# Optimization experiments

Hardware: AMD Instinct MI355X
Metric: run time of the kernel (lower is better)

The kernel has to match this reference:

```python
import jax, jax.numpy as jnp
import numpy as np

N_HEAD = 8
EPS = 1e-6  # LayerNorm2d eps


def setup_inputs() -> dict:
    key = jax.random.key(0)
    ks = jax.random.split(key, 7)
    B, C, H, W = 16, 256, 128, 128
    nh, dk, dv = N_HEAD, 32, 32
    s = 1.0 / np.sqrt(C)
    return {
        "q": jax.random.normal(ks[0], (B, C, H, W), jnp.float32),
        "k": jax.random.normal(ks[1], (B, C, H, W), jnp.float32),
        "v": jax.random.normal(ks[2], (B, C, H, W), jnp.float32),
        # 1x1 convs without bias == channel matmuls; weight shape [out_ch, in_ch]
        "wq": jax.random.normal(ks[3], (nh * dk, C), jnp.float32) * s,
        "wk": jax.random.normal(ks[4], (nh * dk, C), jnp.float32) * s,
        "wv": jax.random.normal(ks[5], (nh * dv, C), jnp.float32) * s,
        "wfc": jax.random.normal(ks[6], (C, nh * dv), jnp.float32) * (1.0 / np.sqrt(nh * dv)),
        "ln_w": jnp.ones((C,), jnp.float32),
        "ln_b": jnp.zeros((C,), jnp.float32),
        "kernel": 5,
        "pad": 2,
    }


def _forward(q, k, v, wq, wk, wv, wfc, ln_w, ln_b, kernel, pad):
    B, C, H, W = q.shape
    nh = N_HEAD
    dk = wq.shape[0] // nh
    dv = wv.shape[0] // nh
    assert kernel == 2 * pad + 1
    residual = q
    # 1x1 conv projections, split into heads: [B, nh, d, H, W]
    qh = jnp.einsum('oc,bchw->bohw', wq, q).reshape(B, nh, dk, H, W)
    kh = jnp.einsum('oc,bchw->bohw', wk, k).reshape(B, nh, dk, H, W)
    vh = jnp.einsum('oc,bchw->bohw', wv, v).reshape(B, nh, dv, H, W)
    # zero-pad spatially: out-of-bounds correlations/values are zero, matching the
    # original bilinear sampler (zeros padding) and the custom padding() helper.
    kp = jnp.pad(kh, ((0, 0), (0, 0), (0, 0), (pad, pad), (pad, pad)))
    vp = jnp.pad(vh, ((0, 0), (0, 0), (0, 0), (pad, pad), (pad, pad)))
    # local correlation volume: dot(q[i,j], k[i+dy-pad, j+dx-pad]) for the KxK window
    # (integer offsets -> bilinear sample degenerates to a gather). Never materializes
    # the full [B, HW, HW] matrix the torch code builds before sampling.
    corr = jnp.stack(
        [jnp.einsum('bncij,bncij->bnij', qh, kp[:, :, :, dy:dy + H, dx:dx + W])
         for dy in range(kernel) for dx in range(kernel)], axis=-1)  # [B,nh,H,W,K*K]
    # relu (from CorrBlock.corr), temperature = sqrt(d_k), softmax over window.
    # OOB entries are 0 (not -inf), faithfully matching the original.
    attn = jax.nn.softmax(jax.nn.relu(corr) / jnp.float32(np.sqrt(dk)), axis=-1)
    # channel attention: per-pixel weighted sum of v over the same window
    out = jnp.zeros((B, nh, dv, H, W), q.dtype)
    idx = 0
    for dy in range(kernel):
        for dx in range(kernel):
            out = out + attn[:, :, :, :, idx][:, :, None] * vp[:, :, :, dy:dy + H, dx:dx + W]
            idx += 1
    o = jnp.einsum('oc,bchw->bohw', wfc, out.reshape(B, nh * dv, H, W)) + residual
    # LayerNorm2d: normalize over channel dim per pixel
    mu = o.mean(1, keepdims=True)
    var = ((o - mu) ** 2).mean(1, keepdims=True)
    y = (o - mu) / jnp.sqrt(var + EPS)
    return ln_w[None, :, None, None] * y + ln_b[None, :, None, None]


def reference(q, k, v, wq, wk, wv, wfc, ln_w, ln_b, kernel, pad):
    return _forward(q, k, v, wq, wk, wv, wfc, ln_w, ln_b, kernel, pad)
```

## Files before the change

kernel.cpp:

```cpp
#include <hip/hip_runtime.h>
#include <hip/hip_bf16.h>

#define BATCH 16
#define CH 256
#define HH 128
#define WW 128
#define HWSZ (HH * WW)
#define NHEAD 8
#define DHEAD 32
#define PW 132
#define PPIX (132 * 132)
#define ROWS 264
#define ASTR 40

typedef __attribute__((ext_vector_type(8))) short bf16x8;
typedef __attribute__((ext_vector_type(4))) float f32x4;
typedef _Float16 h2v __attribute__((ext_vector_type(2)));

__device__ __forceinline__ unsigned short f2h(float f) {
    _Float16 h = (_Float16)f;
    return __builtin_bit_cast(unsigned short, h);
}
__device__ __forceinline__ unsigned pkbf(float a, float b) {
    __hip_bfloat162_raw r = __hip_bfloat162_raw(__float22bfloat162_rn(make_float2(a, b)));
    return (unsigned)r.x | ((unsigned)r.y << 16);
}
__device__ __forceinline__ int swzc(int row, int chunk) { return chunk ^ ((row >> 2) & 7); }

#if __has_builtin(__builtin_amdgcn_fdot2)
#define DOT2(a, b, c) __builtin_amdgcn_fdot2((a), (b), (c), false)
#else
#define DOT2(a, b, c) ((c) + (float)(a)[0] * (float)(b)[0] + (float)(a)[1] * (float)(b)[1])
#endif

__global__ __launch_bounds__(256)
void zpad_kernel(unsigned short* __restrict__ kpad, unsigned short* __restrict__ vpad)
{
    int bid = blockIdx.x;
    unsigned short* dst = ((bid & 1) ? vpad : kpad) + (size_t)(bid >> 1) * PPIX * DHEAD;
    const uint4 z = {0u, 0u, 0u, 0u};
    for (int i = threadIdx.x; i < 1040; i += 256) {
        int row, col;
        if (i < 264)      { row = i / 132; col = i - row * 132; }
        else if (i < 528) { int j = i - 264; int r = j / 132; row = 130 + r; col = j - r * 132; }
        else              { int j = i - 528; row = 2 + (j >> 2); int c = j & 3; col = (c < 2) ? c : (128 + c); }
        uint4* p = reinterpret_cast<uint4*>(dst + (size_t)(row * PW + col) * DHEAD);
        p[0] = z; p[1] = z; p[2] = z; p[3] = z;
    }
}

__global__ __launch_bounds__(256)
void prep_kernel(const float* __restrict__ wq, const float* __restrict__ wk,
                 const float* __restrict__ wv, const float* __restrict__ wfc,
                 unsigned short* __restrict__ wb)
{
    const float* src = (blockIdx.y == 0) ? wq : (blockIdx.y == 1) ? wk
                     : (blockIdx.y == 2) ? wv : wfc;
    unsigned short* dst = wb + blockIdx.y * 65536;
    int e = (blockIdx.x * 256 + threadIdx.x) * 8;
    const float4* s = reinterpret_cast<const float4*>(src + e);
    float4 a = s[0], c = s[1];
    uint4 u;
    u.x = pkbf(a.x, a.y); u.y = pkbf(a.z, a.w);
    u.z = pkbf(c.x, c.y); u.w = pkbf(c.z, c.w);
    *reinterpret_cast<uint4*>(dst + e) = u;
}

__global__ __launch_bounds__(512)
void proj_kernel(const float* __restrict__ q, const float* __restrict__ k,
                 const float* __restrict__ v, const unsigned short* __restrict__ wb,
                 unsigned short* __restrict__ qh, unsigned short* __restrict__ kpad,
                 unsigned short* __restrict__ vpad)
{
    __shared__ __align__(16) unsigned short lB[2][64 * ROWS];

    const int t = threadIdx.x;
    const int z = blockIdx.y;
    const int b = blockIdx.x >> 4;
    const int pt0 = (blockIdx.x & 15) * 16;

    const float* X; unsigned short* Y;
    if (z == 0)      { X = q; Y = qh; }
    else if (z == 1) { X = k; Y = kpad; }
    else             { X = v; Y = vpad; }
    const unsigned short* Wb = wb + z * 65536;
    X += (size_t)b * CH * HWSZ;
    const size_t pixstride = (z == 0) ? (size_t)HWSZ : (size_t)PPIX;
    Y += (size_t)b * NHEAD * pixstride * DHEAD;

    const int lane = t & 63;
    const int wid  = t >> 6;
    const int lrow = lane & 15;
    const int lkg  = lane >> 4;
    const int pxq  = t & 15;
    const int oct  = t >> 4;

    const float* xcol = X + (size_t)(oct * 8) * HWSZ + pxq * 4;

    float4 f[8];
    {
        const float* xb = xcol + pt0 * 64;
#pragma unroll
        for (int i = 0; i < 8; ++i) f[i] = *reinterpret_cast<const float4*>(xb + (size_t)i * HWSZ);
    }
    bf16x8 af[2][8];
#pragma unroll
    for (int m = 0; m < 2; ++m)
#pragma unroll
        for (int ks = 0; ks < 8; ++ks)
            af[m][ks] = *reinterpret_cast<const bf16x8*>(
                Wb + (wid * 32 + m * 16 + lrow) * 256 + ks * 32 + lkg * 8);

#define PACK_LB(BUF) do { \
        uint4 u_; int row_; \
        row_ = pxq * 4 + 0; \
        u_.x = pkbf(f[0].x, f[1].x); u_.y = pkbf(f[2].x, f[3].x); \
        u_.z = pkbf(f[4].x, f[5].x); u_.w = pkbf(f[6].x, f[7].x); \
        *reinterpret_cast<uint4*>(&lB[BUF][row_ * ROWS + swzc(row_, oct) * 8]) = u_; \
        row_ = pxq * 4 + 1; \
        u_.x = pkbf(f[0].y, f[1].y); u_.y = pkbf(f[2].y, f[3].y); \
        u_.z = pkbf(f[4].y, f[5].y); u_.w = pkbf(f[6].y, f[7].y); \
        *reinterpret_cast<uint4*>(&lB[BUF][row_ * ROWS + swzc(row_, oct) * 8]) = u_; \
        row_ = pxq * 4 + 2; \
        u_.x = pkbf(f[0].z, f[1].z); u_.y = pkbf(f[2].z, f[3].z); \
        u_.z = pkbf(f[4].z, f[5].z); u_.w = pkbf(f[6].z, f[7].z); \
        *reinterpret_cast<uint4*>(&lB[BUF][row_ * ROWS + swzc(row_, oct) * 8]) = u_; \
        row_ = pxq * 4 + 3; \
        u_.x = pkbf(f[0].w, f[1].w); u_.y = pkbf(f[2].w, f[3].w); \
        u_.z = pkbf(f[4].w, f[5].w); u_.w = pkbf(f[6].w, f[7].w); \
        *reinterpret_cast<uint4*>(&lB[BUF][row_ * ROWS + swzc(row_, oct) * 8]) = u_; \
    } while (0)

    PACK_LB(0);
    __syncthreads();
    {
        const float* xb = xcol + (pt0 + 1) * 64;
#pragma unroll
        for (int i = 0; i < 8; ++i) f[i] = *reinterpret_cast<const float4*>(xb + (size_t)i * HWSZ);
    }

    for (int it = 0; it < 16; ++it) {
        f32x4 acc[2][4];
        const f32x4 zero = {0.f, 0.f, 0.f, 0.f};
#pragma unroll
        for (int m = 0; m < 2; ++m)
#pragma unroll
            for (int n = 0; n < 4; ++n) acc[m][n] = zero;

#pragma unroll
        for (int ks = 0; ks < 8; ++ks) {
            bf16x8 bfv[4];
#pragma unroll
            for (int n = 0; n < 4; ++n) {
                int row = n * 16 + lrow;
                bfv[n] = *reinterpret_cast<const bf16x8*>(&lB[it & 1][row * ROWS + swzc(row, ks * 4 + lkg) * 8]);
            }
#pragma unroll
            for (int m = 0; m < 2; ++m)
#pragma unroll
                for (int n = 0; n < 4; ++n)
                    acc[m][n] = __builtin_amdgcn_mfma_f32_16x16x32_bf16(af[m][ks], bfv[n], acc[m][n], 0, 0, 0);
        }

        {
            const int p0 = (pt0 + it) * 64;
            const int lr = lane >> 4, lc = lane & 15;
#pragma unroll
            for (int m = 0; m < 2; ++m)
#pragma unroll
                for (int n = 0; n < 4; ++n) {
                    int d0 = m * 16 + lr * 4;
                    int p = p0 + n * 16 + lc;
                    ushort4 pk;
                    pk.x = f2h(acc[m][n][0]); pk.y = f2h(acc[m][n][1]);
                    pk.z = f2h(acc[m][n][2]); pk.w = f2h(acc[m][n][3]);
                    size_t pix;
                    if (z == 0) pix = (size_t)wid * HWSZ + p;
                    else { int row = p >> 7, col = p & 127; pix = (size_t)wid * PPIX + (size_t)(row + 2) * PW + (col + 2); }
                    *reinterpret_cast<ushort4*>(&Y[pix * DHEAD + d0]) = pk;
                }
        }

        if (it + 1 < 16) {
            PACK_LB((it + 1) & 1);
            __syncthreads();
            if (it + 2 < 16) {
                const float* xb = xcol + (pt0 + it + 2) * 64;
#pragma unroll
                for (int i = 0; i < 8; ++i) f[i] = *reinterpret_cast<const float4*>(xb + (size_t)i * HWSZ);
            }
        }
    }
#undef PACK_LB
}

__global__ __launch_bounds__(1024)
void attn_kernel(unsigned short* __restrict__ qh,
                 const unsigned short* __restrict__ kpad,
                 const unsigned short* __restrict__ vpad)
{
    const int t = threadIdx.x;
    const int swz = (blockIdx.x & 7) * 1024 + (blockIdx.x >> 3);
    const int bh = swz >> 6;
    const int tile = swz & 63;
    const int x0 = (tile & 7) * 16, y0 = (tile >> 3) * 16;
    const int qc = t & 3;
    const int px = (t >> 2) & 15;
    const int py = t >> 6;
    const int gx = x0 + px, gy = y0 + py;

    unsigned short* qp = qh + ((size_t)bh * HWSZ + gy * WW + gx) * DHEAD + qc * 8;
    const unsigned short* kb = kpad + (size_t)bh * PPIX * DHEAD + qc * 8;
    const unsigned short* vb = vpad + (size_t)bh * PPIX * DHEAD + qc * 8;

    union { uint4 u; h2v h2[4]; } Q;
    Q.u = *reinterpret_cast<const uint4*>(qp);

    float ew[25];
#pragma unroll
    for (int wy = 0; wy < 5; ++wy) {
        const unsigned short* krow = kb + (size_t)((gy + wy) * PW + gx) * DHEAD;
#pragma unroll
        for (int wx = 0; wx < 5; ++wx) {
            union { uint4 u; h2v h2[4]; } K;
            K.u = *reinterpret_cast<const uint4*>(krow + wx * DHEAD);
            float s = 0.f;
#pragma unroll
            for (int j = 0; j < 4; ++j)
                s = DOT2(Q.h2[j], K.h2[j], s);
            s += __shfl_xor(s, 1);
            s += __shfl_xor(s, 2);
            ew[wy * 5 + wx] = __expf(fmaxf(s, 0.f) * 0.17677669529663687f);
        }
    }

    float sum = 0.f;
#pragma unroll
    for (int i = 0; i < 25; ++i) sum += ew[i];
    const float inv = 1.f / sum;

    union { uint4 u; h2v h2[4]; } A;
    const h2v hz = {(_Float16)0.f, (_Float16)0.f};
#pragma unroll
    for (int j = 0; j < 4; ++j) A.h2[j] = hz;

#pragma unroll
    for (int wy = 0; wy < 5; ++wy) {
        const unsigned short* vrow = vb + (size_t)((gy + wy) * PW + gx) * DHEAD;
#pragma unroll
        for (int wx = 0; wx < 5; ++wx) {
            _Float16 wh = (_Float16)(ew[wy * 5 + wx] * inv);
            h2v w2 = {wh, wh};
            union { uint4 u; h2v h2[4]; } V;
            V.u = *reinterpret_cast<const uint4*>(vrow + wx * DHEAD);
#pragma unroll
            for (int j = 0; j < 4; ++j)
                A.h2[j] += w2 * V.h2[j];
        }
    }

    uint4 o;
    o.x = pkbf((float)A.h2[0][0], (float)A.h2[0][1]);
    o.y = pkbf((float)A.h2[1][0], (float)A.h2[1][1]);
    o.z = pkbf((float)A.h2[2][0], (float)A.h2[2][1]);
    o.w = pkbf((float)A.h2[3][0], (float)A.h2[3][1]);
    *reinterpret_cast<uint4*>(qp) = o;
}

__global__ __launch_bounds__(512)
void fcln_kernel(const unsigned short* __restrict__ ob, const unsigned short* __restrict__ wfcb,
                 const float* __restrict__ qres, const float* __restrict__ lnw,
                 const float* __restrict__ lnb, float* __restrict__ out)
{
    __shared__ __align__(16) unsigned short lB[64 * ROWS];
    __shared__ __align__(16) unsigned short lA[2][256 * ASTR];
    __shared__ float lsum[8][64];
    __shared__ float lssq[8][64];

    const int t = threadIdx.x;
    const int b = blockIdx.y;
    const int p0 = blockIdx.x * 64;

    const int lane = t & 63;
    const int wid  = t >> 6;
    const int lrow = lane & 15;
    const int lkg  = lane >> 4;
    const int ao0 = t >> 1, ak0 = (t & 1) * 2;

#pragma unroll
    for (int r = 0; r < 4; ++r) {
        int idx = r * 512 + t;
        int h = idx >> 8;
        int rem = idx & 255;
        int px = rem >> 2, qc = rem & 3;
        uint4 bv = *reinterpret_cast<const uint4*>(
            ob + ((size_t)(b * NHEAD + h) * HWSZ + p0 + px) * DHEAD + qc * 8);
        *reinterpret_cast<uint4*>(&lB[px * ROWS + swzc(px, h * 4 + qc) * 8]) = bv;
    }
    {
        uint4 w0 = *reinterpret_cast<const uint4*>(wfcb + ao0 * 256 + ak0 * 8);
        uint4 w1 = *reinterpret_cast<const uint4*>(wfcb + ao0 * 256 + ak0 * 8 + 8);
        *reinterpret_cast<uint4*>(&lA[0][ao0 * ASTR + ak0 * 8]) = w0;
        *reinterpret_cast<uint4*>(&lA[0][ao0 * ASTR + ak0 * 8 + 8]) = w1;
    }

    f32x4 acc[2][4];
    const f32x4 zero = {0.f, 0.f, 0.f, 0.f};
#pragma unroll
    for (int m = 0; m < 2; ++m)
#pragma unroll
        for (int n = 0; n < 4; ++n) acc[m][n] = zero;

    __syncthreads();

#pragma unroll
    for (int ks = 0; ks < 8; ++ks) {
        uint4 w0, w1;
        if (ks < 7) {
            w0 = *reinterpret_cast<const uint4*>(wfcb + ao0 * 256 + (ks + 1) * 32 + ak0 * 8);
            w1 = *reinterpret_cast<const uint4*>(wfcb + ao0 * 256 + (ks + 1) * 32 + ak0 * 8 + 8);
        }
        bf16x8 af[2], bfv[4];
#pragma unroll
        for (int m = 0; m < 2; ++m)
            af[m] = *reinterpret_cast<const bf16x8*>(&lA[ks & 1][(wid * 32 + m * 16 + lrow) * ASTR + lkg * 8]);
#pragma unroll
        for (int n = 0; n < 4; ++n) {
            int row = n * 16 + lrow;
            bfv[n] = *reinterpret_cast<const bf16x8*>(&lB[row * ROWS + swzc(row, ks * 4 + lkg) * 8]);
        }
#pragma unroll
        for (int m = 0; m < 2; ++m)
#pragma unroll
            for (int n = 0; n < 4; ++n)
                acc[m][n] = __builtin_amdgcn_mfma_f32_16x16x32_bf16(af[m], bfv[n], acc[m][n], 0, 0, 0);
        if (ks < 7) {
            *reinterpret_cast<uint4*>(&lA[(ks + 1) & 1][ao0 * ASTR + ak0 * 8]) = w0;
            *reinterpret_cast<uint4*>(&lA[(ks + 1) & 1][ao0 * ASTR + ak0 * 8 + 8]) = w1;
            __syncthreads();
        }
    }

    const int lr = lane >> 4, lc = lane & 15;
    const float* qb = qres + (size_t)b * CH * HWSZ;
#pragma unroll
    for (int m = 0; m < 2; ++m)
#pragma unroll
        for (int n = 0; n < 4; ++n)
#pragma unroll
            for (int j = 0; j < 4; ++j) {
                int o = wid * 32 + m * 16 + lr * 4 + j;
                int p = p0 + n * 16 + lc;
                acc[m][n][j] += qb[(size_t)o * HWSZ + p];
            }

    float s[4], s2[4];
#pragma unroll
    for (int n = 0; n < 4; ++n) {
        float a = 0.f, c2 = 0.f;
#pragma unroll
        for (int m = 0; m < 2; ++m)
#pragma unroll
            for (int j = 0; j < 4; ++j) {
                float x = acc[m][n][j];
                a += x; c2 += x * x;
            }
        a  += __shfl_xor(a, 16);  a  += __shfl_xor(a, 32);
        c2 += __shfl_xor(c2, 16); c2 += __shfl_xor(c2, 32);
        s[n] = a; s2[n] = c2;
    }
    __syncthreads();
    if (lane < 16) {
#pragma unroll
        for (int n = 0; n < 4; ++n) {
            lsum[wid][n * 16 + lane] = s[n];
            lssq[wid][n * 16 + lane] = s2[n];
        }
    }
    __syncthreads();

    float mu[4], rs[4];
#pragma unroll
    for (int n = 0; n < 4; ++n) {
        int p = n * 16 + lc;
        float ts = 0.f, tq = 0.f;
#pragma unroll
        for (int w = 0; w < 8; ++w) { ts += lsum[w][p]; tq += lssq[w][p]; }
        float m_ = ts * (1.f / 256.f);
        float v_ = tq * (1.f / 256.f) - m_ * m_;
        mu[n] = m_;
        rs[n] = rsqrtf(v_ + 1e-6f);
    }

    float* op = out + (size_t)b * CH * HWSZ;
#pragma unroll
    for (int m = 0; m < 2; ++m)
#pragma unroll
        for (int j = 0; j < 4; ++j) {
            int o = wid * 32 + m * 16 + lr * 4 + j;
            float g = lnw[o], bb = lnb[o];
#pragma unroll
            for (int n = 0; n < 4; ++n) {
                int p = p0 + n * 16 + lc;
                op[(size_t)o * HWSZ + p] = (acc[m][n][j] - mu[n]) * rs[n] * g + bb;
            }
        }
}

extern "C" void kernel_launch(void* const* d_in, const int* in_sizes, int n_in,
                              void* d_out, int out_size, void* d_ws, size_t ws_size,
                              hipStream_t stream) {
    const float* q   = (const float*)d_in[0];
    const float* k   = (const float*)d_in[1];
    const float* v   = (const float*)d_in[2];
    const float* wq  = (const float*)d_in[3];
    const float* wk  = (const float*)d_in[4];
    const float* wv  = (const float*)d_in[5];
    const float* wfc = (const float*)d_in[6];
    const float* lnw = (const float*)d_in[7];
    const float* lnb = (const float*)d_in[8];

    const size_t qsz = (size_t)BATCH * NHEAD * HWSZ * DHEAD;
    const size_t psz = (size_t)BATCH * NHEAD * PPIX * DHEAD;
    if (ws_size < (qsz + 2 * psz + 4 * 65536) * sizeof(unsigned short)) return;

    unsigned short* qh = (unsigned short*)d_ws;
    unsigned short* kp = qh + qsz;
    unsigned short* vp = kp + psz;
    unsigned short* wb = vp + psz;

    zpad_kernel<<<256, 256, 0, stream>>>(kp, vp);
    prep_kernel<<<dim3(32, 4), 256, 0, stream>>>(wq, wk, wv, wfc, wb);
    proj_kernel<<<dim3(256, 3), 512, 0, stream>>>(q, k, v, wb, qh, kp, vp);
    attn_kernel<<<8192, 1024, 0, stream>>>(qh, kp, vp);
    fcln_kernel<<<dim3(HWSZ / 64, BATCH), 512, 0, stream>>>(qh, wb + 3 * 65536, q, lnw, lnb, (float*)d_out);
}
```

Measured before the change: 690.7 us.

## Fuse local window attention into the output projection and LayerNorm kernel

Merges the attention kernel into the fc+LayerNorm kernel. Each 512-thread block now computes all 8 heads' windowed attention for a 16x8 pixel tile, keeps the results in registers and stages them into LDS in two 64-pixel groups for the MFMA projection. This removes the bf16 round trip of the attention output through global memory and one kernel launch. In exchange each thread loops over 8 heads serially, which raises register pressure. The fc weights are also reloaded for each of the two groups.

```diff
diff --git a/kernel.cpp b/kernel.cpp
--- a/kernel.cpp
+++ b/kernel.cpp
@@ -194,83 +194,13 @@
 #undef PACK_LB
 }
 
-__global__ __launch_bounds__(1024)
-void attn_kernel(unsigned short* __restrict__ qh,
-                 const unsigned short* __restrict__ kpad,
-                 const unsigned short* __restrict__ vpad)
-{
-    const int t = threadIdx.x;
-    const int swz = (blockIdx.x & 7) * 1024 + (blockIdx.x >> 3);
-    const int bh = swz >> 6;
-    const int tile = swz & 63;
-    const int x0 = (tile & 7) * 16, y0 = (tile >> 3) * 16;
-    const int qc = t & 3;
-    const int px = (t >> 2) & 15;
-    const int py = t >> 6;
-    const int gx = x0 + px, gy = y0 + py;
-
-    unsigned short* qp = qh + ((size_t)bh * HWSZ + gy * WW + gx) * DHEAD + qc * 8;
-    const unsigned short* kb = kpad + (size_t)bh * PPIX * DHEAD + qc * 8;
-    const unsigned short* vb = vpad + (size_t)bh * PPIX * DHEAD + qc * 8;
-
-    union { uint4 u; h2v h2[4]; } Q;
-    Q.u = *reinterpret_cast<const uint4*>(qp);
-
-    float ew[25];
-#pragma unroll
-    for (int wy = 0; wy < 5; ++wy) {
-        const unsigned short* krow = kb + (size_t)((gy + wy) * PW + gx) * DHEAD;
-#pragma unroll
-        for (int wx = 0; wx < 5; ++wx) {
-            union { uint4 u; h2v h2[4]; } K;
-            K.u = *reinterpret_cast<const uint4*>(krow + wx * DHEAD);
-            float s = 0.f;
-#pragma unroll
-            for (int j = 0; j < 4; ++j)
-                s = DOT2(Q.h2[j], K.h2[j], s);
-            s += __shfl_xor(s, 1);
-            s += __shfl_xor(s, 2);
-            ew[wy * 5 + wx] = __expf(fmaxf(s, 0.f) * 0.17677669529663687f);
-        }
-    }
-
-    float sum = 0.f;
-#pragma unroll
-    for (int i = 0; i < 25; ++i) sum += ew[i];
-    const float inv = 1.f / sum;
-
-    union { uint4 u; h2v h2[4]; } A;
-    const h2v hz = {(_Float16)0.f, (_Float16)0.f};
-#pragma unroll
-    for (int j = 0; j < 4; ++j) A.h2[j] = hz;
-
-#pragma unroll
-    for (int wy = 0; wy < 5; ++wy) {
-        const unsigned short* vrow = vb + (size_t)((gy + wy) * PW + gx) * DHEAD;
-#pragma unroll
-        for (int wx = 0; wx < 5; ++wx) {
-            _Float16 wh = (_Float16)(ew[wy * 5 + wx] * inv);
-            h2v w2 = {wh, wh};
-            union { uint4 u; h2v h2[4]; } V;
-            V.u = *reinterpret_cast<const uint4*>(vrow + wx * DHEAD);
-#pragma unroll
-            for (int j = 0; j < 4; ++j)
-                A.h2[j] += w2 * V.h2[j];
-        }
-    }
-
-    uint4 o;
-    o.x = pkbf((float)A.h2[0][0], (float)A.h2[0][1]);
-    o.y = pkbf((float)A.h2[1][0], (float)A.h2[1][1]);
-    o.z = pkbf((float)A.h2[2][0], (float)A.h2[2][1]);
-    o.w = pkbf((float)A.h2[3][0], (float)A.h2[3][1]);
-    *reinterpret_cast<uint4*>(qp) = o;
-}
-
 __global__ __launch_bounds__(512)
-void fcln_kernel(const unsigned short* __restrict__ ob, const unsigned short* __restrict__ wfcb,
-                 const float* __restrict__ qres, const float* __restrict__ lnw,
-                 const float* __restrict__ lnb, float* __restrict__ out)
+void attn_fcln_kernel(const unsigned short* __restrict__ qh,
+                      const unsigned short* __restrict__ kpad,
+                      const unsigned short* __restrict__ vpad,
+                      const unsigned short* __restrict__ wfcb,
+                      const float* __restrict__ qres, const float* __restrict__ lnw,
+                      const float* __restrict__ lnb, float* __restrict__ out)
 {
     __shared__ __align__(16) unsigned short lB[64 * ROWS];
     __shared__ __align__(16) unsigned short lA[2][256 * ASTR];
@@ -278,133 +208,202 @@
     __shared__ float lssq[8][64];
 
     const int t = threadIdx.x;
-    const int b = blockIdx.y;
-    const int p0 = blockIdx.x * 64;
+    const int flat = (blockIdx.x & 7) * 256 + (blockIdx.x >> 3);
+    const int b = flat >> 7;
+    const int tile = flat & 127;
+    const int x0 = (tile & 7) * 16, y0 = (tile >> 3) * 8;
+
+    const int px = t >> 2;
+    const int qc = t & 3;
+    const int gx = x0 + (px & 15), gy = y0 + (px >> 4);
+
+    uint4 ah[8];
+#pragma unroll
+    for (int h = 0; h < NHEAD; ++h) {
+        const size_t plane = (size_t)(b * NHEAD + h);
+        const unsigned short* qp = qh + (plane * HWSZ + gy * WW + gx) * DHEAD + qc * 8;
+        const unsigned short* kb = kpad + plane * PPIX * DHEAD + qc * 8;
+        const unsigned short* vb = vpad + plane * PPIX * DHEAD + qc * 8;
+
+        union { uint4 u; h2v h2[4]; } Q;
+        Q.u = *reinterpret_cast<const uint4*>(qp);
+
+        float ew[25];
+#pragma unroll
+        for (int wy = 0; wy < 5; ++wy) {
+            const unsigned short* krow = kb + (size_t)((gy + wy) * PW + gx) * DHEAD;
+#pragma unroll
+            for (int wx = 0; wx < 5; ++wx) {
+                union { uint4 u; h2v h2[4]; } K;
+                K.u = *reinterpret_cast<const uint4*>(krow + wx * DHEAD);
+                float s = 0.f;
+#pragma unroll
+                for (int j = 0; j < 4; ++j)
+                    s = DOT2(Q.h2[j], K.h2[j], s);
+                s += __shfl_xor(s, 1);
+                s += __shfl_xor(s, 2);
+                ew[wy * 5 + wx] = __expf(fmaxf(s, 0.f) * 0.17677669529663687f);
+            }
+        }
+
+        float sum = 0.f;
+#pragma unroll
+        for (int i = 0; i < 25; ++i) sum += ew[i];
+        const float inv = 1.f / sum;
+
+        union { uint4 u; h2v h2[4]; } A;
+        const h2v hz = {(_Float16)0.f, (_Float16)0.f};
+#pragma unroll
+        for (int j = 0; j < 4; ++j) A.h2[j] = hz;
+
+#pragma unroll
+        for (int wy = 0; wy < 5; ++wy) {
+            const unsigned short* vrow = vb + (size_t)((gy + wy) * PW + gx) * DHEAD;
+#pragma unroll
+            for (int wx = 0; wx < 5; ++wx) {
+                _Float16 wh = (_Float16)(ew[wy * 5 + wx] * inv);
+                h2v w2 = {wh, wh};
+                union { uint4 u; h2v h2[4]; } V;
+                V.u = *reinterpret_cast<const uint4*>(vrow + wx * DHEAD);
+#pragma unroll
+                for (int j = 0; j < 4; ++j)
+                    A.h2[j] += w2 * V.h2[j];
+            }
+        }
+
+        uint4 o;
+        o.x = pkbf((float)A.h2[0][0], (float)A.h2[0][1]);
+        o.y = pkbf((float)A.h2[1][0], (float)A.h2[1][1]);
+        o.z = pkbf((float)A.h2[2][0], (float)A.h2[2][1]);
+        o.w = pkbf((float)A.h2[3][0], (float)A.h2[3][1]);
+        ah[h] = o;
+    }
 
     const int lane = t & 63;
     const int wid  = t >> 6;
     const int lrow = lane & 15;
     const int lkg  = lane >> 4;
     const int ao0 = t >> 1, ak0 = (t & 1) * 2;
-
-#pragma unroll
-    for (int r = 0; r < 4; ++r) {
-        int idx = r * 512 + t;
-        int h = idx >> 8;
-        int rem = idx & 255;
-        int px = rem >> 2, qc = rem & 3;
-        uint4 bv = *reinterpret_cast<const uint4*>(
-            ob + ((size_t)(b * NHEAD + h) * HWSZ + p0 + px) * DHEAD + qc * 8);
-        *reinterpret_cast<uint4*>(&lB[px * ROWS + swzc(px, h * 4 + qc) * 8]) = bv;
-    }
-    {
-        uint4 w0 = *reinterpret_cast<const uint4*>(wfcb + ao0 * 256 + ak0 * 8);
-        uint4 w1 = *reinterpret_cast<const uint4*>(wfcb + ao0 * 256 + ak0 * 8 + 8);
-        *reinterpret_cast<uint4*>(&lA[0][ao0 * ASTR + ak0 * 8]) = w0;
-        *reinterpret_cast<uint4*>(&lA[0][ao0 * ASTR + ak0 * 8 + 8]) = w1;
-    }
-
-    f32x4 acc[2][4];
-    const f32x4 zero = {0.f, 0.f, 0.f, 0.f};
-#pragma unroll
-    for (int m = 0; m < 2; ++m)
-#pragma unroll
-        for (int n = 0; n < 4; ++n) acc[m][n] = zero;
-
-    __syncthreads();
-
-#pragma unroll
-    for (int ks = 0; ks < 8; ++ks) {
-        uint4 w0, w1;
-        if (ks < 7) {
-            w0 = *reinterpret_cast<const uint4*>(wfcb + ao0 * 256 + (ks + 1) * 32 + ak0 * 8);
-            w1 = *reinterpret_cast<const uint4*>(wfcb + ao0 * 256 + (ks + 1) * 32 + ak0 * 8 + 8);
-        }
-        bf16x8 af[2], bfv[4];
+    const float* qb = qres + (size_t)b * CH * HWSZ;
+    float* opb = out + (size_t)b * CH * HWSZ;
+
+    for (int g = 0; g < 2; ++g) {
+        __syncthreads();
+
+        if ((px >> 6) == g) {
+            int r = px & 63;
+#pragma unroll
+            for (int h = 0; h < NHEAD; ++h)
+                *reinterpret_cast<uint4*>(&lB[r * ROWS + swzc(r, h * 4 + qc) * 8]) = ah[h];
+        }
+        {
+            uint4 w0 = *reinterpret_cast<const uint4*>(wfcb + ao0 * 256 + ak0 * 8);
+            uint4 w1 = *reinterpret_cast<const uint4*>(wfcb + ao0 * 256 + ak0 * 8 + 8);
+            *reinterpret_cast<uint4*>(&lA[0][ao0 * ASTR + ak0 * 8]) = w0;
+            *reinterpret_cast<uint4*>(&lA[0][ao0 * ASTR + ak0 * 8 + 8]) = w1;
+        }
+
+        f32x4 acc[2][4];
+        const f32x4 zero = {0.f, 0.f, 0.f, 0.f};
 #pragma unroll
         for (int m = 0; m < 2; ++m)
-            af[m] = *reinterpret_cast<const bf16x8*>(&lA[ks & 1][(wid * 32 + m * 16 + lrow) * ASTR + lkg * 8]);
+#pragma unroll
+            for (int n = 0; n < 4; ++n) acc[m][n] = zero;
+
+        __syncthreads();
+
+#pragma unroll
+        for (int ks = 0; ks < 8; ++ks) {
+            uint4 w0, w1;
+            if (ks < 7) {
+                w0 = *reinterpret_cast<const uint4*>(wfcb + ao0 * 256 + (ks + 1) * 32 + ak0 * 8);
+                w1 = *reinterpret_cast<const uint4*>(wfcb + ao0 * 256 + (ks + 1) * 32 + ak0 * 8 + 8);
+            }
+            bf16x8 af[2], bfv[4];
+#pragma unroll
+            for (int m = 0; m < 2; ++m)
+                af[m] = *reinterpret_cast<const bf16x8*>(&lA[ks & 1][(wid * 32 + m * 16 + lrow) * ASTR + lkg * 8]);
+#pragma unroll
+            for (int n = 0; n < 4; ++n) {
+                int row = n * 16 + lrow;
+                bfv[n] = *reinterpret_cast<const bf16x8*>(&lB[row * ROWS + swzc(row, ks * 4 + lkg) * 8]);
+            }
+#pragma unroll
+            for (int m = 0; m < 2; ++m)
+#pragma unroll
+                for (int n = 0; n < 4; ++n)
+                    acc[m][n] = __builtin_amdgcn_mfma_f32_16x16x32_bf16(af[m], bfv[n], acc[m][n], 0, 0, 0);
+            if (ks < 7) {
+                *reinterpret_cast<uint4*>(&lA[(ks + 1) & 1][ao0 * ASTR + ak0 * 8]) = w0;
+                *reinterpret_cast<uint4*>(&lA[(ks + 1) & 1][ao0 * ASTR + ak0 * 8 + 8]) = w1;
+                __syncthreads();
+            }
+        }
+
+        const int lr = lane >> 4, lc = lane & 15;
+#pragma unroll
+        for (int m = 0; m < 2; ++m)
+#pragma unroll
+            for (int n = 0; n < 4; ++n) {
+                int p = (y0 + g * 4 + n) * WW + x0 + lc;
+#pragma unroll
+                for (int j = 0; j < 4; ++j) {
+                    int o = wid * 32 + m * 16 + lr * 4 + j;
+                    acc[m][n][j] += qb[(size_t)o * HWSZ + p];
+                }
+            }
+
+        float s[4], s2[4];
 #pragma unroll
         for (int n = 0; n < 4; ++n) {
-            int row = n * 16 + lrow;
-            bfv[n] = *reinterpret_cast<const bf16x8*>(&lB[row * ROWS + swzc(row, ks * 4 + lkg) * 8]);
-        }
+            float a = 0.f, c2 = 0.f;
+#pragma unroll
+            for (int m = 0; m < 2; ++m)
+#pragma unroll
+                for (int j = 0; j < 4; ++j) {
+                    float x = acc[m][n][j];
+                    a += x; c2 += x * x;
+                }
+            a  += __shfl_xor(a, 16);  a  += __shfl_xor(a, 32);
+            c2 += __shfl_xor(c2, 16); c2 += __shfl_xor(c2, 32);
+            s[n] = a; s2[n] = c2;
+        }
+        __syncthreads();
+        if (lane < 16) {
+#pragma unroll
+            for (int n = 0; n < 4; ++n) {
+                lsum[wid][n * 16 + lane] = s[n];
+                lssq[wid][n * 16 + lane] = s2[n];
+            }
+        }
+        __syncthreads();
+
+        float mu[4], rs[4];
+#pragma unroll
+        for (int n = 0; n < 4; ++n) {
+            int pp = n * 16 + lc;
+            float ts = 0.f, tq = 0.f;
+#pragma unroll
+            for (int w = 0; w < 8; ++w) { ts += lsum[w][pp]; tq += lssq[w][pp]; }
+            float m_ = ts * (1.f / 256.f);
+            float v_ = tq * (1.f / 256.f) - m_ * m_;
+            mu[n] = m_;
+            rs[n] = rsqrtf(v_ + 1e-6f);
+        }
+
 #pragma unroll
         for (int m = 0; m < 2; ++m)
-#pragma unroll
-            for (int n = 0; n < 4; ++n)
-                acc[m][n] = __builtin_amdgcn_mfma_f32_16x16x32_bf16(af[m], bfv[n], acc[m][n], 0, 0, 0);
-        if (ks < 7) {
-            *reinterpret_cast<uint4*>(&lA[(ks + 1) & 1][ao0 * ASTR + ak0 * 8]) = w0;
-            *reinterpret_cast<uint4*>(&lA[(ks + 1) & 1][ao0 * ASTR + ak0 * 8 + 8]) = w1;
-            __syncthreads();
-        }
-    }
-
-    const int lr = lane >> 4, lc = lane & 15;
-    const float* qb = qres + (size_t)b * CH * HWSZ;
-#pragma unroll
-    for (int m = 0; m < 2; ++m)
-#pragma unroll
-        for (int n = 0; n < 4; ++n)
 #pragma unroll
             for (int j = 0; j < 4; ++j) {
                 int o = wid * 32 + m * 16 + lr * 4 + j;
-                int p = p0 + n * 16 + lc;
-                acc[m][n][j] += qb[(size_t)o * HWSZ + p];
-            }
-
-    float s[4], s2[4];
-#pragma unroll
-    for (int n = 0; n < 4; ++n) {
-        float a = 0.f, c2 = 0.f;
-#pragma unroll
-        for (int m = 0; m < 2; ++m)
-#pragma unroll
-            for (int j = 0; j < 4; ++j) {
-                float x = acc[m][n][j];
-                a += x; c2 += x * x;
-            }
-        a  += __shfl_xor(a, 16);  a  += __shfl_xor(a, 32);
-        c2 += __shfl_xor(c2, 16); c2 += __shfl_xor(c2, 32);
-        s[n] = a; s2[n] = c2;
-    }
-    __syncthreads();
-    if (lane < 16) {
-#pragma unroll
-        for (int n = 0; n < 4; ++n) {
-            lsum[wid][n * 16 + lane] = s[n];
-            lssq[wid][n * 16 + lane] = s2[n];
-        }
-    }
-    __syncthreads();
-
-    float mu[4], rs[4];
-#pragma unroll
-    for (int n = 0; n < 4; ++n) {
-        int p = n * 16 + lc;
-        float ts = 0.f, tq = 0.f;
-#pragma unroll
-        for (int w = 0; w < 8; ++w) { ts += lsum[w][p]; tq += lssq[w][p]; }
-        float m_ = ts * (1.f / 256.f);
-        float v_ = tq * (1.f / 256.f) - m_ * m_;
-        mu[n] = m_;
-        rs[n] = rsqrtf(v_ + 1e-6f);
-    }
-
-    float* op = out + (size_t)b * CH * HWSZ;
-#pragma unroll
-    for (int m = 0; m < 2; ++m)
-#pragma unroll
-        for (int j = 0; j < 4; ++j) {
-            int o = wid * 32 + m * 16 + lr * 4 + j;
-            float g = lnw[o], bb = lnb[o];
-#pragma unroll
-            for (int n = 0; n < 4; ++n) {
-                int p = p0 + n * 16 + lc;
-                op[(size_t)o * HWSZ + p] = (acc[m][n][j] - mu[n]) * rs[n] * g + bb;
-            }
-        }
+                float gw = lnw[o], bb = lnb[o];
+#pragma unroll
+                for (int n = 0; n < 4; ++n) {
+                    int p = (y0 + g * 4 + n) * WW + x0 + lc;
+                    opb[(size_t)o * HWSZ + p] = (acc[m][n][j] - mu[n]) * rs[n] * gw + bb;
+                }
+            }
+    }
 }
 
 extern "C" void kernel_launch(void* const* d_in, const int* in_sizes, int n_in,
@@ -432,6 +431,5 @@
     zpad_kernel<<<256, 256, 0, stream>>>(kp, vp);
     prep_kernel<<<dim3(32, 4), 256, 0, stream>>>(wq, wk, wv, wfc, wb);
     proj_kernel<<<dim3(256, 3), 512, 0, stream>>>(q, k, v, wb, qh, kp, vp);
-    attn_kernel<<<8192, 1024, 0, stream>>>(qh, kp, vp);
-    fcln_kernel<<<dim3(HWSZ / 64, BATCH), 512, 0, stream>>>(qh, wb + 3 * 65536, q, lnw, lnb, (float*)d_out);
-}
+    attn_fcln_kernel<<<2048, 512, 0, stream>>>(qh, kp, vp, wb + 3 * 65536, q, lnw, lnb, (float*)d_out);
+}
```

Result: slower. 931.4 us (+34.8%).
